# Kernel optimization log

Measured on AMD Instinct MI355X. Metric: run time of the kernel, lower is better.

## Reference

```python
import jax, jax.numpy as jnp
import numpy as np

C = 256
EPS = 1e-5


def setup_inputs() -> dict:
    key = jax.random.key(0)
    ks = jax.random.split(key, 10)
    B, H, W = 4, 64, 64
    x1 = jax.random.normal(ks[0], (B, C, H, W), dtype=jnp.float32)
    x2 = jax.random.normal(ks[1], (B, C, H, W), dtype=jnp.float32)
    s = 1.0 / np.sqrt(C)
    qw = jax.random.normal(ks[2], (C, C), dtype=jnp.float32) * s
    qb = jax.random.normal(ks[3], (C,), dtype=jnp.float32) * 0.01
    kw = jax.random.normal(ks[4], (C, C), dtype=jnp.float32) * s
    kb = jax.random.normal(ks[5], (C,), dtype=jnp.float32) * 0.01
    vw = jax.random.normal(ks[6], (C, C), dtype=jnp.float32) * s
    vb = jax.random.normal(ks[7], (C,), dtype=jnp.float32) * 0.01
    ln_w = jnp.ones((C,), dtype=jnp.float32)
    ln_b = jnp.zeros((C,), dtype=jnp.float32)
    return {"x1": x1, "x2": x2, "qw": qw, "qb": qb, "kw": kw, "kb": kb,
            "vw": vw, "vb": vb, "ln_w": ln_w, "ln_b": ln_b}


def _conv1x1(x, w, b):
    # 1x1 conv == per-pixel matmul over channels. x: [B,C,H,W], w: [O,C]
    return jnp.einsum('oc,bchw->bohw', w, x) + b[None, :, None, None]


def reference(x1, x2, qw, qb, kw, kb, vw, vb, ln_w, ln_b):
    q = _conv1x1(x1, qw, qb)   # [B,C,H,W]
    k = _conv1x1(x2, kw, kb)   # [B,C,H,W]
    v = _conv1x1(x2, vw, vb)   # [B,C,H,W]
    # scores: [B,H,W,I,J]; softmax over LAST axis (j) only, as in the torch code
    scores = jnp.einsum('bchw,bcij->bhwij', q, k)
    attn = jax.nn.softmax(scores, axis=-1)
    fusion = jnp.einsum('bhwij,bcij->bchw', attn, v)  # [B,C,H,W]
    # LayerNorm2d: normalize over channel dim per spatial location
    mean = jnp.mean(fusion, axis=1, keepdims=True)
    var = jnp.var(fusion, axis=1, keepdims=True)
    normed = (fusion - mean) * jax.lax.rsqrt(var + EPS)
    return normed * ln_w[None, :, None, None] + ln_b[None, :, None, None]
```

## Files before the change

### kernel.cpp

```cpp
#include <hip/hip_runtime.h>


#define CDIM 256
#define NPOS 4096
#define BATCH 4
#define EPSV 1e-5f

typedef _Float16 f16;
typedef __attribute__((ext_vector_type(4))) _Float16 f16x4;
typedef __attribute__((ext_vector_type(8))) _Float16 f16x8;
typedef __attribute__((ext_vector_type(4))) float f32x4;
typedef __attribute__((ext_vector_type(16))) float f32x16;

#define WST       264
#define QK_STRIDE 264
#define V_STRIDE  72
#define DQ_STRIDE 72
#define FM_STRIDE 36

#define LBAR() asm volatile("s_waitcnt lgkmcnt(0)\n\ts_barrier" ::: "memory")


static __device__ __forceinline__ f16x8 cvt8(const float* __restrict__ p) {
    float4 w0 = *(const float4*)p;
    float4 w1 = *(const float4*)(p + 4);
    f16x8 r;
    r[0] = (f16)w0.x; r[1] = (f16)w0.y; r[2] = (f16)w0.z; r[3] = (f16)w0.w;
    r[4] = (f16)w1.x; r[5] = (f16)w1.y; r[6] = (f16)w1.z; r[7] = (f16)w1.w;
    return r;
}

__global__ __launch_bounds__(256, 4) void wconv_kernel(
    const float* __restrict__ qw, const float* __restrict__ kw,
    const float* __restrict__ vw, f16* __restrict__ Wf)
{
    const int id = blockIdx.x;
    const int t  = threadIdx.x;
    const int pr = id >> 3;
    const int q  = (id >> 1) & 3;
    const int ot = id & 1;
    const float* W = (pr == 0 ? qw : pr == 1 ? kw : vw);
    f16* D = Wf + (size_t)id * 8192;
    #pragma unroll
    for (int i = 0; i < 4; ++i) {
        int idx = t + i * 256;
        int ks = idx >> 6, l = idx & 63;
        const float* src = W + (size_t)(q * 64 + ot * 32 + (l & 31)) * CDIM
                             + ks * 16 + (l >> 5) * 8;
        *(f16x8*)(D + (size_t)idx * 8) = cvt8(src);
    }
}

__global__ __launch_bounds__(256, 3) void gemm_kernel(
    const float* __restrict__ x1, const float* __restrict__ x2,
    const f16* __restrict__ Wf,
    const float* __restrict__ qb, const float* __restrict__ kb,
    const float* __restrict__ vb,
    f16* __restrict__ Qg, f16* __restrict__ Kg, f16* __restrict__ Vg)
{
    __shared__ f16 Xs[64 * WST];
    __shared__ f16 Ds[64 * DQ_STRIDE];
    __shared__ float biasS[256];

    const int id = blockIdx.x;
    const int pr  = id >> 8;
    const int rem = id & 255;
    const int b   = rem >> 6;
    const int p0  = (rem & 63) << 6;
    const float* xsrc = ((pr == 0) ? x1 : x2) + (size_t)b * CDIM * NPOS + p0;
    const float* bias = (pr == 0) ? qb : (pr == 1) ? kb : vb;

    const int t = threadIdx.x, w = t >> 6, l = t & 63, lm = l & 31, lh = l >> 5;
    const int pt = w & 1, ot = w >> 1;

    const f16* Wfp = Wf + (size_t)pr * 65536 + (size_t)ot * 8192;

    biasS[t] = bias[t];
    #pragma unroll
    for (int g = 0; g < 8; ++g) {
        f16x8 h;
        #pragma unroll
        for (int j = 0; j < 8; ++j)
            h[j] = (f16)xsrc[(size_t)(w * 64 + g * 8 + j) * NPOS + l];
        *(f16x8*)&Xs[l * WST + w * 64 + g * 8] = h;
    }

    f16x8 wf[16];
    #pragma unroll
    for (int ks = 0; ks < 16; ++ks)
        wf[ks] = *(const f16x8*)(Wfp + (size_t)ks * 512 + l * 8);

    __syncthreads();

    for (int q = 0; q < 4; ++q) {
        f32x16 accA = {}, accB = {};
        #pragma unroll
        for (int ks = 0; ks < 16; ks += 2) {
            f16x8 x0  = *(const f16x8*)&Xs[(pt * 32 + lm) * WST + ks * 16 + lh * 8];
            f16x8 x1v = *(const f16x8*)&Xs[(pt * 32 + lm) * WST + (ks + 1) * 16 + lh * 8];
            if (pr < 2) {
                accA = __builtin_amdgcn_mfma_f32_32x32x16_f16(x0, wf[ks], accA, 0, 0, 0);
                accB = __builtin_amdgcn_mfma_f32_32x32x16_f16(x1v, wf[ks + 1], accB, 0, 0, 0);
            } else {
                accA = __builtin_amdgcn_mfma_f32_32x32x16_f16(wf[ks], x0, accA, 0, 0, 0);
                accB = __builtin_amdgcn_mfma_f32_32x32x16_f16(wf[ks + 1], x1v, accB, 0, 0, 0);
            }
        }

        if (q < 3) {
            #pragma unroll
            for (int ks = 0; ks < 16; ++ks)
                wf[ks] = *(const f16x8*)(Wfp + (size_t)(q + 1) * 16384
                                             + (size_t)ks * 512 + l * 8);
        }

        if (pr < 2) {
            int o_l = ot * 32 + lm;
            float bv = biasS[q * 64 + o_l];
            #pragma unroll
            for (int r = 0; r < 16; ++r) {
                int p_l = pt * 32 + (r & 3) + 8 * (r >> 2) + 4 * lh;
                Ds[p_l * DQ_STRIDE + o_l] = (f16)(accA[r] + accB[r] + bv);
            }
        } else {
            #pragma unroll
            for (int r = 0; r < 16; ++r) {
                int o_l = ot * 32 + (r & 3) + 8 * (r >> 2) + 4 * lh;
                Ds[o_l * DQ_STRIDE + pt * 32 + lm] =
                    (f16)(accA[r] + accB[r] + biasS[q * 64 + o_l]);
            }
        }
        LBAR();

        #pragma unroll
        for (int j = 0; j < 2; ++j) {
            int row = (t >> 3) + j * 32;
            int cc  = (t & 7) * 8;
            f16x8 vdat = *(const f16x8*)&Ds[row * DQ_STRIDE + cc];
            if (pr < 2) {
                f16* Out = (pr == 0) ? Qg : Kg;
                *(f16x8*)(Out + ((size_t)(b * NPOS + p0 + row)) * CDIM + q * 64 + cc) = vdat;
            } else {
                *(f16x8*)(Vg + ((size_t)(b * CDIM + q * 64 + row)) * NPOS + p0 + cc) = vdat;
            }
        }
        LBAR();
    }
}

__global__ __launch_bounds__(256, 2) void attn_kernel(
    const f16* __restrict__ Qg, const f16* __restrict__ Kg, const f16* __restrict__ Vg,
    float* __restrict__ Fp)
{
    __shared__ f16   Ks[64 * QK_STRIDE];
    __shared__ f16   Vs[256 * V_STRIDE];
    __shared__ f16   Pl[64 * V_STRIDE];
    __shared__ float RedM[2][64], RedS[2][64];

    const int t    = threadIdx.x;
    const int L    = (int)((blockIdx.x & 7) * 64 + (blockIdx.x >> 3));
    const int grp  = L >> 6;
    const int b    = grp >> 1;
    const int half = grp & 1;
    const int qt   = L & 63;
    const int p0   = qt << 6;
    const int bq   = b * 64 + qt;
    const int w    = t >> 6;
    const int l    = t & 63;
    const int lm   = l & 31;
    const int lh   = l >> 5;
    const int spt  = w & 1;
    const int skt  = w >> 1;

    f16x8 qf[16];
    {
        const f16* qptr = Qg + (size_t)(b * NPOS + p0 + spt * 32 + lm) * CDIM + lh * 8;
        #pragma unroll
        for (int ks = 0; ks < 16; ++ks) qf[ks] = *(const f16x8*)(qptr + ks * 16);
    }

    const int kr = t >> 5, koff = (t & 31) * 8;
    f16x8 kreg[8];
    auto issue_k = [&](int ch) {
        const int i0 = ch * 64;
        #pragma unroll
        for (int r = 0; r < 8; ++r)
            kreg[r] = *(const f16x8*)(Kg + (size_t)(b * NPOS + i0 + r * 8 + kr) * CDIM + koff);
    };

    const int vr = t >> 3;
    const int vc = (t & 7) * 8;
    f16x8 vreg[8];
    auto issue_v = [&](int ch) {
        const int i0 = ch * 64;
        #pragma unroll
        for (int i = 0; i < 8; ++i)
            vreg[i] = *(const f16x8*)(Vg + (size_t)(b * CDIM + i * 32 + vr) * NPOS + i0 + vc);
    };

    issue_k(half * 32);
    issue_v(half * 32);

    f32x16 facc[4] = {};

    for (int it = 0; it < 32; ++it) {
        const int ch = half * 32 + it;

        #pragma unroll
        for (int r = 0; r < 8; ++r)
            *(f16x8*)&Ks[(r * 8 + kr) * QK_STRIDE + koff] = kreg[r];
        if (it < 31) issue_k(ch + 1);
        LBAR();

        #pragma unroll
        for (int i = 0; i < 8; ++i)
            *(f16x8*)&Vs[(i * 32 + vr) * V_STRIDE + vc] = vreg[i];
        if (it < 31) issue_v(ch + 1);

        f32x16 st = {};
        __builtin_amdgcn_s_setprio(1);
        #pragma unroll
        for (int ks = 0; ks < 16; ++ks) {
            f16x8 kf = *(const f16x8*)&Ks[(skt * 32 + lm) * QK_STRIDE + ks * 16 + lh * 8];
            st = __builtin_amdgcn_mfma_f32_32x32x16_f16(kf, qf[ks], st, 0, 0, 0);
        }
        __builtin_amdgcn_s_setprio(0);

        float mx = st[0];
        #pragma unroll
        for (int r = 1; r < 16; ++r) mx = fmaxf(mx, st[r]);
        mx = fmaxf(mx, __shfl_xor(mx, 32));
        float ss = 0.f;
        #pragma unroll
        for (int r = 0; r < 16; ++r) {
            float e = __expf(st[r] - mx);
            st[r] = e;
            ss += e;
        }
        ss += __shfl_xor(ss, 32);
        if (lh == 0) { RedM[skt][spt * 32 + lm] = mx; RedS[skt][spt * 32 + lm] = ss; }
        LBAR();

        float mo = RedM[skt ^ 1][spt * 32 + lm];
        float so = RedS[skt ^ 1][spt * 32 + lm];
        float M  = fmaxf(mx, mo);
        float S  = ss * __expf(mx - M) + so * __expf(mo - M);
        float scale = __expf(mx - M) * __builtin_amdgcn_rcpf(S);

        #pragma unroll
        for (int rq = 0; rq < 4; ++rq) {
            f16x4 pk;
            #pragma unroll
            for (int q2 = 0; q2 < 4; ++q2) pk[q2] = (f16)(st[rq * 4 + q2] * scale);
            *(f16x4*)&Pl[(spt * 32 + lm) * V_STRIDE + skt * 32 + rq * 8 + lh * 4] = pk;
        }
        LBAR();

        __builtin_amdgcn_s_setprio(1);
        #pragma unroll
        for (int kb = 0; kb < 4; ++kb) {
            f16x8 pf0 = *(const f16x8*)&Pl[lm * V_STRIDE + kb * 16 + lh * 8];
            f16x8 pf1 = *(const f16x8*)&Pl[(32 + lm) * V_STRIDE + kb * 16 + lh * 8];
            f16x8 va0 = *(const f16x8*)&Vs[(w * 64 + lm) * V_STRIDE + kb * 16 + lh * 8];
            f16x8 va1 = *(const f16x8*)&Vs[(w * 64 + 32 + lm) * V_STRIDE + kb * 16 + lh * 8];
            facc[0] = __builtin_amdgcn_mfma_f32_32x32x16_f16(va0, pf0, facc[0], 0, 0, 0);
            facc[1] = __builtin_amdgcn_mfma_f32_32x32x16_f16(va0, pf1, facc[1], 0, 0, 0);
            facc[2] = __builtin_amdgcn_mfma_f32_32x32x16_f16(va1, pf0, facc[2], 0, 0, 0);
            facc[3] = __builtin_amdgcn_mfma_f32_32x32x16_f16(va1, pf1, facc[3], 0, 0, 0);
        }
        __builtin_amdgcn_s_setprio(0);
    }

    float* dst = Fp + ((size_t)bq * 2 + half) * (CDIM * 64);
    #pragma unroll
    for (int ii = 0; ii < 2; ++ii)
        #pragma unroll
        for (int jj = 0; jj < 2; ++jj)
            #pragma unroll
            for (int r = 0; r < 16; ++r) {
                int c = w * 64 + ii * 32 + (r & 3) + 8 * (r >> 2) + 4 * lh;
                int p = jj * 32 + lm;
                dst[c * 64 + p] = facc[ii * 2 + jj][r];
            }
}

__global__ __launch_bounds__(256, 2) void merge_ln_kernel(
    const float* __restrict__ Fp, const float* __restrict__ ln_w,
    const float* __restrict__ ln_b, float* __restrict__ out)
{
    __shared__ float Fs[256 * FM_STRIDE];
    __shared__ float redS[32 * 32], redQ[32 * 32];
    __shared__ float lnw_s[256], lnb_s[256];
    __shared__ float mu_s[32], rs_s[32];

    const int t  = threadIdx.x;
    const int bq = blockIdx.x >> 1;
    const int ph = blockIdx.x & 1;
    const int b  = bq >> 6;
    const int p0 = (bq & 63) * 64 + ph * 32;

    lnw_s[t] = ln_w[t]; lnb_s[t] = ln_b[t];

    const int pb = (t & 7) * 4;
    const int cg = t >> 3;
    const float* base = Fp + (size_t)bq * 2 * (CDIM * 64) + ph * 32;

    f32x4 s4 = {}, q4 = {};
    #pragma unroll
    for (int ci = 0; ci < 8; ++ci) {
        int c = cg * 8 + ci;
        size_t off = (size_t)c * 64 + pb;
        f32x4 v = *(const f32x4*)(base + off);
        v += *(const f32x4*)(base + (size_t)(CDIM * 64) + off);
        *(f32x4*)&Fs[c * FM_STRIDE + pb] = v;
        s4 += v; q4 += v * v;
    }
    #pragma unroll
    for (int k2 = 0; k2 < 4; ++k2) {
        redS[cg * 32 + pb + k2] = s4[k2];
        redQ[cg * 32 + pb + k2] = q4[k2];
    }
    __syncthreads();
    if (t < 32) {
        float ss = 0.f, qq = 0.f;
        #pragma unroll
        for (int g2 = 0; g2 < 32; ++g2) { ss += redS[g2 * 32 + t]; qq += redQ[g2 * 32 + t]; }
        float mean = ss * (1.0f / 256.0f);
        float var  = qq * (1.0f / 256.0f) - mean * mean;
        mu_s[t] = mean;
        rs_s[t] = rsqrtf(var + EPSV);
    }
    __syncthreads();
    const int p   = t & 31;
    const int cg2 = t >> 5;
    const float mu = mu_s[p], rs = rs_s[p];
    float* dst = out + (size_t)b * CDIM * NPOS + p0 + p;
    #pragma unroll 4
    for (int ci = 0; ci < 32; ++ci) {
        int c = cg2 * 32 + ci;
        dst[(size_t)c * NPOS] = (Fs[c * FM_STRIDE + p] - mu) * rs * lnw_s[c] + lnb_s[c];
    }
}

extern "C" void kernel_launch(void* const* d_in, const int* in_sizes, int n_in,
                              void* d_out, int out_size, void* d_ws, size_t ws_size,
                              hipStream_t stream)
{
    const float* x1  = (const float*)d_in[0];
    const float* x2  = (const float*)d_in[1];
    const float* qw  = (const float*)d_in[2];
    const float* qb  = (const float*)d_in[3];
    const float* kw  = (const float*)d_in[4];
    const float* kb  = (const float*)d_in[5];
    const float* vw  = (const float*)d_in[6];
    const float* vb  = (const float*)d_in[7];
    const float* lnw = (const float*)d_in[8];
    const float* lnb = (const float*)d_in[9];

    const size_t tsz = (size_t)BATCH * NPOS * CDIM;
    f16* Qg  = (f16*)d_ws;
    f16* Kg  = Qg + tsz;
    f16* Vg  = Kg + tsz;
    f16* Wf  = Vg + tsz;
    float* Fp = (float*)(Wf + 3 * CDIM * CDIM);

    wconv_kernel<<<24, 256, 0, stream>>>(qw, kw, vw, Wf);
    gemm_kernel<<<768, 256, 0, stream>>>(x1, x2, Wf, qb, kb, vb, Qg, Kg, Vg);
    attn_kernel<<<512, 256, 0, stream>>>(Qg, Kg, Vg, Fp);
    merge_ln_kernel<<<512, 256, 0, stream>>>(Fp, lnw, lnb, (float*)d_out);
}
```

Before: 208.4 us.

## Store V in MFMA fragment layout and load directly to registers; double-buffer K

The projection kernel now writes V in a pre-swizzled per-tile MFMA fragment order, so the attention kernel can load each wave's V operands straight from global memory into registers. This drops the shared-memory V staging and one barrier per iteration. K staging moves to a double-buffered shared array so the next chunk is written while the current one is consumed. In exchange, the V loads now sit right before their use with less latency hiding, and shared memory per block changes (the V buffer is removed and K doubles).

```diff
diff --git a/kernel.cpp b/kernel.cpp
--- a/kernel.cpp
+++ b/kernel.cpp
@@ -56,7 +56,7 @@
     const f16* __restrict__ Wf,
     const float* __restrict__ qb, const float* __restrict__ kb,
     const float* __restrict__ vb,
-    f16* __restrict__ Qg, f16* __restrict__ Kg, f16* __restrict__ Vg)
+    f16* __restrict__ Qg, f16* __restrict__ Kg, f16* __restrict__ Vf)
 {
     __shared__ f16 Xs[64 * WST];
     __shared__ f16 Ds[64 * DQ_STRIDE];
@@ -132,16 +132,27 @@
         }
         LBAR();
 
-        #pragma unroll
-        for (int j = 0; j < 2; ++j) {
-            int row = (t >> 3) + j * 32;
-            int cc  = (t & 7) * 8;
-            f16x8 vdat = *(const f16x8*)&Ds[row * DQ_STRIDE + cc];
-            if (pr < 2) {
+        if (pr < 2) {
+            #pragma unroll
+            for (int j = 0; j < 2; ++j) {
+                int row = (t >> 3) + j * 32;
+                int cc  = (t & 7) * 8;
+                f16x8 vdat = *(const f16x8*)&Ds[row * DQ_STRIDE + cc];
                 f16* Out = (pr == 0) ? Qg : Kg;
                 *(f16x8*)(Out + ((size_t)(b * NPOS + p0 + row)) * CDIM + q * 64 + cc) = vdat;
-            } else {
-                *(f16x8*)(Vg + ((size_t)(b * CDIM + q * 64 + row)) * NPOS + p0 + cc) = vdat;
+            }
+        } else {
+            #pragma unroll
+            for (int i = 0; i < 2; ++i) {
+                int idx  = t + i * 256;
+                int ct_l = idx >> 8;
+                int kb_  = (idx >> 6) & 3;
+                int l2   = idx & 63;
+                f16x8 vdat = *(const f16x8*)&Ds[(ct_l * 32 + (l2 & 31)) * DQ_STRIDE +
+                                                kb_ * 16 + (l2 >> 5) * 8];
+                size_t fo = ((((size_t)b * 64 + (p0 >> 6)) * 8 + q * 2 + ct_l) * 4 + kb_) * 512
+                            + l2 * 8;
+                *(f16x8*)(Vf + fo) = vdat;
             }
         }
         LBAR();
@@ -149,11 +160,10 @@
 }
 
 __global__ __launch_bounds__(256, 2) void attn_kernel(
-    const f16* __restrict__ Qg, const f16* __restrict__ Kg, const f16* __restrict__ Vg,
+    const f16* __restrict__ Qg, const f16* __restrict__ Kg, const f16* __restrict__ Vf,
     float* __restrict__ Fp)
 {
-    __shared__ f16   Ks[64 * QK_STRIDE];
-    __shared__ f16   Vs[256 * V_STRIDE];
+    __shared__ f16   Ks[2][64 * QK_STRIDE];
     __shared__ f16   Pl[64 * V_STRIDE];
     __shared__ float RedM[2][64], RedS[2][64];
 
@@ -188,40 +198,41 @@
             kreg[r] = *(const f16x8*)(Kg + (size_t)(b * NPOS + i0 + r * 8 + kr) * CDIM + koff);
     };
 
-    const int vr = t >> 3;
-    const int vc = (t & 7) * 8;
-    f16x8 vreg[8];
-    auto issue_v = [&](int ch) {
-        const int i0 = ch * 64;
-        #pragma unroll
-        for (int i = 0; i < 8; ++i)
-            vreg[i] = *(const f16x8*)(Vg + (size_t)(b * CDIM + i * 32 + vr) * NPOS + i0 + vc);
-    };
+    const f16* Vfb = Vf + (size_t)b * 64 * 8 * 4 * 512;
 
     issue_k(half * 32);
-    issue_v(half * 32);
+    #pragma unroll
+    for (int r = 0; r < 8; ++r)
+        *(f16x8*)&Ks[0][(r * 8 + kr) * QK_STRIDE + koff] = kreg[r];
+    issue_k(half * 32 + 1);
+    LBAR();
 
     f32x16 facc[4] = {};
 
     for (int it = 0; it < 32; ++it) {
         const int ch = half * 32 + it;
-
-        #pragma unroll
-        for (int r = 0; r < 8; ++r)
-            *(f16x8*)&Ks[(r * 8 + kr) * QK_STRIDE + koff] = kreg[r];
-        if (it < 31) issue_k(ch + 1);
-        LBAR();
-
-        #pragma unroll
-        for (int i = 0; i < 8; ++i)
-            *(f16x8*)&Vs[(i * 32 + vr) * V_STRIDE + vc] = vreg[i];
-        if (it < 31) issue_v(ch + 1);
+        const int cb = it & 1;
+
+        const f16* Vt = Vfb + (size_t)ch * 8 * 4 * 512;
+        f16x8 vf0[4], vf1[4];
+        #pragma unroll
+        for (int kb = 0; kb < 4; ++kb) {
+            vf0[kb] = *(const f16x8*)(Vt + (size_t)((2 * w) * 4 + kb) * 512 + l * 8);
+            vf1[kb] = *(const f16x8*)(Vt + (size_t)((2 * w + 1) * 4 + kb) * 512 + l * 8);
+        }
+
+        if (it < 31) {
+            #pragma unroll
+            for (int r = 0; r < 8; ++r)
+                *(f16x8*)&Ks[cb ^ 1][(r * 8 + kr) * QK_STRIDE + koff] = kreg[r];
+            if (it < 30) issue_k(ch + 2);
+        }
 
         f32x16 st = {};
         __builtin_amdgcn_s_setprio(1);
         #pragma unroll
         for (int ks = 0; ks < 16; ++ks) {
-            f16x8 kf = *(const f16x8*)&Ks[(skt * 32 + lm) * QK_STRIDE + ks * 16 + lh * 8];
+            f16x8 kf = *(const f16x8*)&Ks[cb][(skt * 32 + lm) * QK_STRIDE + ks * 16 + lh * 8];
             st = __builtin_amdgcn_mfma_f32_32x32x16_f16(kf, qf[ks], st, 0, 0, 0);
         }
         __builtin_amdgcn_s_setprio(0);
@@ -261,12 +272,10 @@
         for (int kb = 0; kb < 4; ++kb) {
             f16x8 pf0 = *(const f16x8*)&Pl[lm * V_STRIDE + kb * 16 + lh * 8];
             f16x8 pf1 = *(const f16x8*)&Pl[(32 + lm) * V_STRIDE + kb * 16 + lh * 8];
-            f16x8 va0 = *(const f16x8*)&Vs[(w * 64 + lm) * V_STRIDE + kb * 16 + lh * 8];
-            f16x8 va1 = *(const f16x8*)&Vs[(w * 64 + 32 + lm) * V_STRIDE + kb * 16 + lh * 8];
-            facc[0] = __builtin_amdgcn_mfma_f32_32x32x16_f16(va0, pf0, facc[0], 0, 0, 0);
-            facc[1] = __builtin_amdgcn_mfma_f32_32x32x16_f16(va0, pf1, facc[1], 0, 0, 0);
-            facc[2] = __builtin_amdgcn_mfma_f32_32x32x16_f16(va1, pf0, facc[2], 0, 0, 0);
-            facc[3] = __builtin_amdgcn_mfma_f32_32x32x16_f16(va1, pf1, facc[3], 0, 0, 0);
+            facc[0] = __builtin_amdgcn_mfma_f32_32x32x16_f16(vf0[kb], pf0, facc[0], 0, 0, 0);
+            facc[1] = __builtin_amdgcn_mfma_f32_32x32x16_f16(vf0[kb], pf1, facc[1], 0, 0, 0);
+            facc[2] = __builtin_amdgcn_mfma_f32_32x32x16_f16(vf1[kb], pf0, facc[2], 0, 0, 0);
+            facc[3] = __builtin_amdgcn_mfma_f32_32x32x16_f16(vf1[kb], pf1, facc[3], 0, 0, 0);
         }
         __builtin_amdgcn_s_setprio(0);
     }
@@ -360,12 +369,12 @@
     const size_t tsz = (size_t)BATCH * NPOS * CDIM;
     f16* Qg  = (f16*)d_ws;
     f16* Kg  = Qg + tsz;
-    f16* Vg  = Kg + tsz;
-    f16* Wf  = Vg + tsz;
+    f16* Vf  = Kg + tsz;
+    f16* Wf  = Vf + tsz;
     float* Fp = (float*)(Wf + 3 * CDIM * CDIM);
 
     wconv_kernel<<<24, 256, 0, stream>>>(qw, kw, vw, Wf);
-    gemm_kernel<<<768, 256, 0, stream>>>(x1, x2, Wf, qb, kb, vb, Qg, Kg, Vg);
-    attn_kernel<<<512, 256, 0, stream>>>(Qg, Kg, Vg, Fp);
+    gemm_kernel<<<768, 256, 0, stream>>>(x1, x2, Wf, qb, kb, vb, Qg, Kg, Vf);
+    attn_kernel<<<512, 256, 0, stream>>>(Qg, Kg, Vf, Fp);
     merge_ln_kernel<<<512, 256, 0, stream>>>(Fp, lnw, lnb, (float*)d_out);
 }
```

Result: faster. 201.0 us (-3.5%).
